# Optimization experiments

Hardware: AMD Instinct MI355X
Metric: run time of the kernel (lower is better)

## Reference

```python
import jax, jax.numpy as jnp
import numpy as np

B, L, D, H = 2, 128, 256, 256
BASE_LR = 0.01
LR_SHIFT = float(np.log(np.expm1(BASE_LR)))  # log(expm1(base_lr))


def silu_backward(x):
    s = jax.nn.silu(x)
    return s + jax.nn.sigmoid(x) * (1.0 - s)


def decay_matrix(log_g):
    # log_g: [B,L] -> M[b,l,m] = exp(sum_{i=m+1..l} log_g[b,i]) for m<=l, else 0
    n = log_g.shape[1]
    strict = jnp.tril(jnp.ones((n, n), log_g.dtype), -1)
    cum = jnp.cumsum(log_g[:, :, None] * strict, axis=1)
    return jnp.exp(cum) * jnp.tril(jnp.ones((n, n), log_g.dtype))


def setup_inputs():
    key = jax.random.key(0)
    ks = jax.random.split(key, 22)
    p = lambda k, shape: jax.random.normal(k, shape, jnp.float32) * 0.02
    inp = {
        'x': jax.random.normal(ks[0], (B, L, D), jnp.float32),
        'Wq': p(ks[1], (D, D)), 'bq': p(ks[2], (D,)),
        'Wk': p(ks[3], (D, D)), 'bk': p(ks[4], (D,)),
        'Wv': p(ks[5], (D, D)), 'bv': p(ks[6], (D,)),
        'Wlr': p(ks[7], (D, 1)), 'blr': p(ks[8], (1,)),
        'Wm': p(ks[9], (D, 1)), 'bm': p(ks[10], (1,)),
        'Wd': p(ks[11], (D, 1)), 'bd': p(ks[12], (1,)),
        'W1': p(ks[13], (B, H, D)), 'b1': p(ks[14], (B, H)),
        'W2': p(ks[15], (B, D, H)), 'b2': p(ks[16], (B, D)),
        'mW1': p(ks[17], (B, H, D)), 'mb1': p(ks[18], (B, H)),
        'mW2': p(ks[19], (B, D, H)), 'mb2': p(ks[20], (B, D)),
    }
    return inp


def reference(x, Wq, bq, Wk, bk, Wv, bv, Wlr, blr, Wm, bm, Wd, bd,
              W1, b1, W2, b2, mW1, mb1, mW2, mb2):
    query = x @ Wq + bq
    key_ = x @ Wk + bk
    value = x @ Wv + bv

    # forward through fast-weight MLP at current (chunk-start) weights
    Z1 = jnp.einsum('bhd,bld->blh', W1, key_) + b1[:, None, :]
    X2 = jax.nn.silu(Z1)
    Z2 = jnp.einsum('bdh,blh->bld', W2, X2) + b2[:, None, :]

    # per-token gradients of 0.5*||Z2 - value||^2
    grad_Z2 = Z2 - value
    grad_b2 = grad_Z2
    grad_W2 = jnp.einsum('bld,blh->bldh', grad_Z2, X2)
    grad_X2 = jnp.einsum('bld,bdh->blh', grad_Z2, W2)
    grad_Z1 = grad_X2 * silu_backward(Z1)
    grad_b1 = grad_Z1
    grad_W1 = jnp.einsum('blh,bld->blhd', grad_Z1, key_)

    lr = jax.nn.softplus((x @ Wlr).squeeze(-1) + blr + LR_SHIFT)  # [B,L]
    gW1 = grad_W1 * lr[:, :, None, None]
    gb1 = grad_b1 * lr[:, :, None]
    gW2 = grad_W2 * lr[:, :, None, None]
    gb2 = grad_b2 * lr[:, :, None]

    # momentum recurrence (decay-gated linear scan, materialized as LxL matrix)
    fc_mom = (x @ Wm).squeeze(-1) + bm  # [B,L]
    log_mom = -jax.nn.softplus(-fc_mom)
    M = decay_matrix(log_mom)  # [B,L,L]
    mom_cum = jnp.exp(jnp.cumsum(log_mom, axis=1))  # [B,L]

    mgW1 = jnp.einsum('blm,bmhd->blhd', M, gW1) - jnp.einsum('bl,bhd->blhd', mom_cum, mW1)
    mgb1 = jnp.einsum('blm,bmh->blh', M, gb1) - jnp.einsum('bl,bh->blh', mom_cum, mb1)
    mgW2 = jnp.einsum('blm,bmdh->bldh', M, gW2) - jnp.einsum('bl,bdh->bldh', mom_cum, mW2)
    mgb2 = jnp.einsum('blm,bmd->bld', M, gb2) - jnp.einsum('bl,bd->bld', mom_cum, mb2)

    # weight-decay recurrence
    log_wd = -jax.nn.softplus((x @ Wd).squeeze(-1) + bd)  # [B,L]
    Dm = decay_matrix(log_wd)
    wd_cum = jnp.exp(jnp.cumsum(log_wd, axis=1))

    W1p = jnp.einsum('blm,bmhd->blhd', Dm, mgW1) + jnp.einsum('bl,bhd->blhd', wd_cum, W1)
    b1p = jnp.einsum('blm,bmh->blh', Dm, mgb1) + jnp.einsum('bl,bh->blh', wd_cum, b1)
    W2p = jnp.einsum('blm,bmdh->bldh', Dm, mgW2) + jnp.einsum('bl,bdh->bldh', wd_cum, W2)
    b2p = jnp.einsum('blm,bmd->bld', Dm, mgb2) + jnp.einsum('bl,bd->bld', wd_cum, b2)

    # query pass through per-token updated weights
    Zq1 = jnp.einsum('blhd,bld->blh', W1p, query) + b1p
    Zq2 = jnp.einsum('bldh,blh->bld', W2p, jax.nn.silu(Zq1)) + b2p

    return (Zq2,
            W1p[:, -1], b1p[:, -1], W2p[:, -1], b2p[:, -1],
            mgW1[:, -1], mgb1[:, -1], mgW2[:, -1], mgb2[:, -1])
```

## Files before the change

### kernel.cpp

```cpp
#include <hip/hip_runtime.h>
#include <hip/hip_bf16.h>
#include <math.h>

constexpr int Bn = 2, Ln = 128, Dn = 256, Hn = 256;

#define LR_SHIFT (-4.6001660040607144f)

constexpr int OFF_Q      = 0;
constexpr int OFF_K      = 65536;
constexpr int OFF_V      = 131072;
constexpr int OFF_X2     = 196608;
constexpr int OFF_SILD   = 262144;
constexpr int OFF_XQ     = 327680;
constexpr int OFF_KT     = 393216;
constexpr int OFF_X2T    = 458752;
constexpr int OFF_A      = 524288;
constexpr int OFF_B1CAT  = 557056;
constexpr int OFF_B2CAT  = 884736;
constexpr int OFF_A1CAT  = 1212416;
constexpr int OFF_A2CAT  = 1376256;
constexpr int OFF_FC     = 1540096;
constexpr int OFF_LR     = 1540864;
constexpr int OFF_PM     = 1541120;
constexpr int OFF_PD     = 1541376;
constexpr int OFF_MOMCUM = 1541632;
constexpr int OFF_WDCUM  = 1541888;
constexpr int OFF_C      = 1542144;
constexpr int OFF_WCAT   = OFF_A1CAT;

constexpr int OUT_ZQ2  = 0;
constexpr int OUT_W1P  = 65536;
constexpr int OUT_B1P  = 196608;
constexpr int OUT_W2P  = 197120;
constexpr int OUT_B2P  = 328192;
constexpr int OUT_MGW1 = 328704;
constexpr int OUT_MGB1 = 459776;
constexpr int OUT_MGW2 = 460288;
constexpr int OUT_MGB2 = 591360;

__device__ __forceinline__ float softplus_f(float z) {
    return fmaxf(z, 0.0f) + log1pf(expf(-fabsf(z)));
}

__device__ __forceinline__ void gemm_mainloop(
    const float* __restrict__ A, int lda,
    const float* __restrict__ B, int ldb, int K,
    float4& c0, float4& c1) {
    __shared__ float As[32][34];
    __shared__ float Bs[32][64];
    const int t = threadIdx.x;
    const int tx = t & 15, ty = t >> 4;
    const int am = t >> 3, ak4 = (t & 7) << 2;
    const int bk = t >> 4, bn4 = (t & 15) << 2;
    c0 = make_float4(0.f, 0.f, 0.f, 0.f);
    c1 = make_float4(0.f, 0.f, 0.f, 0.f);
    for (int kc = 0; kc < K; kc += 32) {
        float4 ga  = *(const float4*)(A + am * lda + kc + ak4);
        float4 gb0 = *(const float4*)(B + (kc + bk) * ldb + bn4);
        float4 gb1 = *(const float4*)(B + (kc + bk + 16) * ldb + bn4);
        __syncthreads();
        As[ak4 + 0][am] = ga.x; As[ak4 + 1][am] = ga.y;
        As[ak4 + 2][am] = ga.z; As[ak4 + 3][am] = ga.w;
        *(float4*)&Bs[bk][bn4]      = gb0;
        *(float4*)&Bs[bk + 16][bn4] = gb1;
        __syncthreads();
#pragma unroll
        for (int k = 0; k < 32; ++k) {
            float a0 = As[k][2 * ty], a1 = As[k][2 * ty + 1];
            float4 b4 = *(const float4*)&Bs[k][4 * tx];
            c0.x += a0 * b4.x; c0.y += a0 * b4.y; c0.z += a0 * b4.z; c0.w += a0 * b4.w;
            c1.x += a1 * b4.x; c1.y += a1 * b4.y; c1.z += a1 * b4.z; c1.w += a1 * b4.w;
        }
    }
}

__global__ __launch_bounds__(256) void repack_kernel(
    const float* __restrict__ Wq, const float* __restrict__ Wk,
    const float* __restrict__ Wv, const float* __restrict__ Wlr,
    const float* __restrict__ Wm, const float* __restrict__ Wd,
    float* __restrict__ ws) {
    int d = blockIdx.x, t = threadIdx.x;
    float* row = ws + OFF_WCAT + d * 832;
    row[t]       = Wq[d * 256 + t];
    row[256 + t] = Wk[d * 256 + t];
    row[512 + t] = Wv[d * 256 + t];
    if (t == 0) { row[768] = Wlr[d]; row[769] = Wm[d]; row[770] = Wd[d]; }
    if (t < 61) row[771 + t] = 0.0f;
}

__global__ __launch_bounds__(256) void transpose_kernel(
    const float* __restrict__ W1, const float* __restrict__ W2,
    const float* __restrict__ mW1, const float* __restrict__ mW2,
    float* __restrict__ ws) {
    int z = blockIdx.z; int mat = z >> 1; int b = z & 1;
    const float* src; float* dst;
    if (mat == 0)      { src = W1  + b * 65536; dst = ws + OFF_B1CAT + b * 163840 + 128 * 256; }
    else if (mat == 1) { src = W2  + b * 65536; dst = ws + OFF_B2CAT + b * 163840 + 128 * 256; }
    else if (mat == 2) { src = mW1 + b * 65536; dst = ws + OFF_B1CAT + b * 163840 + 384 * 256; }
    else               { src = mW2 + b * 65536; dst = ws + OFF_B2CAT + b * 163840 + 384 * 256; }
    __shared__ float tile[32][33];
    int tx = threadIdx.x & 31, ty = threadIdx.x >> 5;
    int r0 = blockIdx.y * 32, c0 = blockIdx.x * 32;
    for (int i = 0; i < 32; i += 8)
        tile[ty + i][tx] = src[(r0 + ty + i) * 256 + (c0 + tx)];
    __syncthreads();
    for (int i = 0; i < 32; i += 8)
        dst[(c0 + ty + i) * 256 + (r0 + tx)] = tile[tx][ty + i];
}

__global__ __launch_bounds__(256) void qkv_kernel(
    const float* __restrict__ x, const float* __restrict__ bq,
    const float* __restrict__ bkb, const float* __restrict__ bv,
    float* __restrict__ ws) {
    int colT = blockIdx.x, rowT = blockIdx.y;
    const float* A = x + rowT * 32 * 256;
    const float* B = ws + OFF_WCAT + colT * 64;
    float4 c0, c1;
    gemm_mainloop(A, 256, B, 832, 256, c0, c1);
    int tx = threadIdx.x & 15, ty = threadIdx.x >> 4;
    float cc[2][4] = {{c0.x, c0.y, c0.z, c0.w}, {c1.x, c1.y, c1.z, c1.w}};
#pragma unroll
    for (int i = 0; i < 2; ++i)
#pragma unroll
        for (int j = 0; j < 4; ++j) {
            int m = rowT * 32 + 2 * ty + i;
            int c = colT * 64 + 4 * tx + j;
            float v = cc[i][j];
            if (c < 256) {
                ws[OFF_Q + m * 256 + c] = v + bq[c];
            } else if (c < 512) {
                int d = c - 256; float kv = v + bkb[d];
                ws[OFF_K + m * 256 + d] = kv;
                ws[OFF_KT + (m >> 7) * 32768 + d * 128 + (m & 127)] = kv;
            } else if (c < 768) {
                ws[OFF_V + m * 256 + (c - 512)] = v + bv[c - 512];
            } else if (c == 768) ws[OFF_FC + m] = v;
            else if (c == 769) ws[OFF_FC + 256 + m] = v;
            else if (c == 770) ws[OFF_FC + 512 + m] = v;
        }
}

__global__ __launch_bounds__(128) void scan_kernel(
    const float* __restrict__ blr, const float* __restrict__ bm,
    const float* __restrict__ bd, float* __restrict__ ws) {
    int b = blockIdx.x, t = threadIdx.x;
    int m = b * 128 + t;
    ws[OFF_LR + m] = softplus_f(ws[OFF_FC + m] + blr[0] + LR_SHIFT);
    float lm = -softplus_f(-(ws[OFF_FC + 256 + m] + bm[0]));
    float ld = -softplus_f(ws[OFF_FC + 512 + m] + bd[0]);
    __shared__ float sm[128], sd[128], se[128];
    sm[t] = lm; sd[t] = ld;
    __syncthreads();
    for (int off = 1; off < 128; off <<= 1) {
        float am = (t >= off) ? sm[t - off] : 0.0f;
        float ad = (t >= off) ? sd[t - off] : 0.0f;
        __syncthreads();
        sm[t] += am; sd[t] += ad;
        __syncthreads();
    }
    float pm = sm[t], pd = sd[t];
    ws[OFF_PM + m] = pm;
    ws[OFF_PD + m] = pd;
    ws[OFF_MOMCUM + m] = expf(pm);
    ws[OFF_WDCUM + m]  = expf(pd);
    se[t] = expf(pm - pd);
    __syncthreads();
    for (int off = 1; off < 128; off <<= 1) {
        float a = (t >= off) ? se[t - off] : 0.0f;
        __syncthreads();
        se[t] += a;
        __syncthreads();
    }
    ws[OFF_C + m] = expf(pd) * se[t];
}

__global__ __launch_bounds__(256) void a_kernel(float* __restrict__ ws) {
    int bl = blockIdx.x, b = bl >> 7, l = bl & 127, t = threadIdx.x;
    const float* Pm = ws + OFF_PM + b * 128;
    const float* Pd = ws + OFF_PD + b * 128;
    if (t < 128) {
        float a = 0.0f;
        if (t <= l) {
            float pdl = Pd[l], pmm1 = Pm[t], s = 0.0f;
            for (int mm = t; mm <= l; ++mm)
                s += expf((pdl - Pd[mm]) + (Pm[mm] - pmm1));
            a = s;
        }
        ws[OFF_A + bl * 128 + t] = a;
    }
    float q  = ws[OFF_Q + bl * 256 + t];
    float wd = ws[OFF_WDCUM + b * 128 + l];
    float cl = ws[OFF_C + b * 128 + l];
    float* A1 = ws + OFF_A1CAT + b * 81920 + l * 640;
    A1[128 + t] = wd * q;
    A1[384 + t] = -cl * q;
}

__global__ __launch_bounds__(256) void z1_kernel(
    const float* __restrict__ b1, float* __restrict__ ws) {
    int colT = blockIdx.x, rowT = blockIdx.y, b = blockIdx.z;
    const float* A = ws + OFF_K + b * 32768 + rowT * 32 * 256;
    const float* B = ws + OFF_B1CAT + b * 163840 + 128 * 256 + colT * 64;
    float4 c0, c1;
    gemm_mainloop(A, 256, B, 256, 256, c0, c1);
    int tx = threadIdx.x & 15, ty = threadIdx.x >> 4;
    float cc[2][4] = {{c0.x, c0.y, c0.z, c0.w}, {c1.x, c1.y, c1.z, c1.w}};
#pragma unroll
    for (int i = 0; i < 2; ++i)
#pragma unroll
        for (int j = 0; j < 4; ++j) {
            int ml = rowT * 32 + 2 * ty + i;
            int n = colT * 64 + 4 * tx + j;
            float z = cc[i][j] + b1[b * 256 + n];
            float sg = 1.0f / (1.0f + expf(-z));
            float x2 = z * sg;
            int gm = b * 128 + ml;
            ws[OFF_X2 + gm * 256 + n] = x2;
            ws[OFF_X2T + b * 32768 + n * 128 + ml] = x2;
            ws[OFF_SILD + gm * 256 + n] = x2 + sg * (1.0f - x2);
        }
}

__global__ __launch_bounds__(256) void z2_kernel(
    const float* __restrict__ b2, float* __restrict__ ws) {
    int colT = blockIdx.x, rowT = blockIdx.y, b = blockIdx.z;
    const float* A = ws + OFF_X2 + b * 32768 + rowT * 32 * 256;
    const float* B = ws + OFF_B2CAT + b * 163840 + 128 * 256 + colT * 64;
    float4 c0, c1;
    gemm_mainloop(A, 256, B, 256, 256, c0, c1);
    int tx = threadIdx.x & 15, ty = threadIdx.x >> 4;
    float cc[2][4] = {{c0.x, c0.y, c0.z, c0.w}, {c1.x, c1.y, c1.z, c1.w}};
#pragma unroll
    for (int i = 0; i < 2; ++i)
#pragma unroll
        for (int j = 0; j < 4; ++j) {
            int ml = rowT * 32 + 2 * ty + i;
            int n = colT * 64 + 4 * tx + j;
            int gm = b * 128 + ml;
            float gz2 = cc[i][j] + b2[b * 256 + n] - ws[OFF_V + gm * 256 + n];
            ws[OFF_B2CAT + b * 163840 + ml * 256 + n] = gz2;
        }
}

__global__ __launch_bounds__(256) void gx2_kernel(
    const float* __restrict__ W2, float* __restrict__ ws) {
    int colT = blockIdx.x, rowT = blockIdx.y, b = blockIdx.z;
    const float* A = ws + OFF_B2CAT + b * 163840 + rowT * 32 * 256;
    const float* B = W2 + b * 65536 + colT * 64;
    float4 c0, c1;
    gemm_mainloop(A, 256, B, 256, 256, c0, c1);
    int tx = threadIdx.x & 15, ty = threadIdx.x >> 4;
    float cc[2][4] = {{c0.x, c0.y, c0.z, c0.w}, {c1.x, c1.y, c1.z, c1.w}};
#pragma unroll
    for (int i = 0; i < 2; ++i)
#pragma unroll
        for (int j = 0; j < 4; ++j) {
            int ml = rowT * 32 + 2 * ty + i;
            int n = colT * 64 + 4 * tx + j;
            int gm = b * 128 + ml;
            float gz1 = cc[i][j] * ws[OFF_SILD + gm * 256 + n];
            ws[OFF_B1CAT + b * 163840 + ml * 256 + n] = gz1;
        }
}

__global__ __launch_bounds__(256) void score_kernel(
    const float* __restrict__ Arows, const float* __restrict__ Bt,
    float* __restrict__ Acat, const float* __restrict__ ws) {
    int colT = blockIdx.x, rowT = blockIdx.y, b = blockIdx.z;
    int tx = threadIdx.x & 15, ty = threadIdx.x >> 4;
    if (colT * 64 > rowT * 32 + 31) {
#pragma unroll
        for (int i = 0; i < 2; ++i)
#pragma unroll
            for (int j = 0; j < 4; ++j) {
                int l = rowT * 32 + 2 * ty + i;
                int mc = colT * 64 + 4 * tx + j;
                Acat[b * 81920 + l * 640 + mc] = 0.0f;
            }
        return;
    }
    const float* A = Arows + b * 32768 + rowT * 32 * 256;
    const float* B = Bt + b * 32768 + colT * 64;
    float4 c0, c1;
    gemm_mainloop(A, 256, B, 128, 256, c0, c1);
    float cc[2][4] = {{c0.x, c0.y, c0.z, c0.w}, {c1.x, c1.y, c1.z, c1.w}};
#pragma unroll
    for (int i = 0; i < 2; ++i)
#pragma unroll
        for (int j = 0; j < 4; ++j) {
            int l = rowT * 32 + 2 * ty + i;
            int mc = colT * 64 + 4 * tx + j;
            float p = 0.0f;
            if (mc <= l)
                p = ws[OFF_A + (b * 128 + l) * 128 + mc] *
                    ws[OFF_LR + b * 128 + mc] * (1.0f + cc[i][j]);
            Acat[b * 81920 + l * 640 + mc] = p;
        }
}

__global__ __launch_bounds__(256) void zq1_kernel(
    const float* __restrict__ b1, const float* __restrict__ mb1,
    float* __restrict__ ws) {
    int colT = blockIdx.x, rowT = blockIdx.y, b = blockIdx.z;
    const float* A = ws + OFF_A1CAT + b * 81920 + rowT * 32 * 640;
    const float* B = ws + OFF_B1CAT + b * 163840 + colT * 64;
    float4 c0, c1;
    gemm_mainloop(A, 640, B, 256, 640, c0, c1);
    int tx = threadIdx.x & 15, ty = threadIdx.x >> 4;
    float cc[2][4] = {{c0.x, c0.y, c0.z, c0.w}, {c1.x, c1.y, c1.z, c1.w}};
#pragma unroll
    for (int i = 0; i < 2; ++i)
#pragma unroll
        for (int j = 0; j < 4; ++j) {
            int ml = rowT * 32 + 2 * ty + i;
            int n = colT * 64 + 4 * tx + j;
            float cl = ws[OFF_C + b * 128 + ml];
            float wd = ws[OFF_WDCUM + b * 128 + ml];
            float z = cc[i][j] + wd * b1[b * 256 + n] - cl * mb1[b * 256 + n];
            float sg = 1.0f / (1.0f + expf(-z));
            float xq = z * sg;
            ws[OFF_XQ + (b * 128 + ml) * 256 + n] = xq;
            float* A2 = ws + OFF_A2CAT + b * 81920 + ml * 640;
            A2[128 + n] = wd * xq;
            A2[384 + n] = -cl * xq;
        }
}

__global__ __launch_bounds__(256) void zq2_kernel(
    const float* __restrict__ b2, const float* __restrict__ mb2,
    float* __restrict__ out, float* __restrict__ ws) {
    int colT = blockIdx.x, rowT = blockIdx.y, b = blockIdx.z;
    const float* A = ws + OFF_A2CAT + b * 81920 + rowT * 32 * 640;
    const float* B = ws + OFF_B2CAT + b * 163840 + colT * 64;
    float4 c0, c1;
    gemm_mainloop(A, 640, B, 256, 640, c0, c1);
    int tx = threadIdx.x & 15, ty = threadIdx.x >> 4;
    float cc[2][4] = {{c0.x, c0.y, c0.z, c0.w}, {c1.x, c1.y, c1.z, c1.w}};
#pragma unroll
    for (int i = 0; i < 2; ++i)
#pragma unroll
        for (int j = 0; j < 4; ++j) {
            int ml = rowT * 32 + 2 * ty + i;
            int n = colT * 64 + 4 * tx + j;
            float cl = ws[OFF_C + b * 128 + ml];
            float wd = ws[OFF_WDCUM + b * 128 + ml];
            out[OUT_ZQ2 + (b * 128 + ml) * 256 + n] =
                cc[i][j] + wd * b2[b * 256 + n] - cl * mb2[b * 256 + n];
        }
}

__global__ __launch_bounds__(256) void lastw_kernel(
    const float* __restrict__ W1, const float* __restrict__ mW1,
    const float* __restrict__ W2, const float* __restrict__ mW2,
    const float* __restrict__ ws, float* __restrict__ out) {
    int z = blockIdx.z; int b = z >> 1; int fam = z & 1;
    int t = threadIdx.x;
    __shared__ float wa[128], wm[128];
    __shared__ float LA[128][16], LM[128][16], R[128][16];
    const float* lr = ws + OFF_LR + b * 128;
    const float* Pm = ws + OFF_PM + b * 128;
    const float* Arow = ws + OFF_A + (b * 128 + 127) * 128;
    if (t < 128) {
        wa[t] = Arow[t] * lr[t];
        wm[t] = expf(Pm[127] - Pm[t]) * lr[t];
    }
    const float* left  = ws + (fam == 0 ? OFF_B1CAT : OFF_B2CAT) + b * 163840;
    const float* right = ws + (fam == 0 ? OFF_K : OFF_X2) + b * 32768;
    int i0 = blockIdx.y * 16, j0 = blockIdx.x * 16;
    __syncthreads();
    for (int e = t; e < 2048; e += 256) {
        int m = e >> 4, i = e & 15;
        float lv = left[m * 256 + i0 + i];
        LA[m][i] = wa[m] * lv;
        LM[m][i] = wm[m] * lv;
        R[m][i]  = right[m * 256 + j0 + i];
    }
    __syncthreads();
    int tx = t & 15, ty = t >> 4;
    float accA = 0.0f, accM = 0.0f;
#pragma unroll 4
    for (int m = 0; m < 128; ++m) {
        accA += LA[m][ty] * R[m][tx];
        accM += LM[m][ty] * R[m][tx];
    }
    float c_last  = ws[OFF_C + b * 128 + 127];
    float wd_last = ws[OFF_WDCUM + b * 128 + 127];
    float mc_last = ws[OFF_MOMCUM + b * 128 + 127];
    int i = i0 + ty, j = j0 + tx;
    const float* base1 = (fam == 0 ? W1 : W2) + b * 65536;
    const float* basem = (fam == 0 ? mW1 : mW2) + b * 65536;
    float b1v = base1[i * 256 + j], bmv = basem[i * 256 + j];
    int op = (fam == 0 ? OUT_W1P : OUT_W2P) + (b * 256 + i) * 256 + j;
    int om = (fam == 0 ? OUT_MGW1 : OUT_MGW2) + (b * 256 + i) * 256 + j;
    out[op] = accA - c_last * bmv + wd_last * b1v;
    out[om] = accM - mc_last * bmv;
}

__global__ __launch_bounds__(256) void lastb_kernel(
    const float* __restrict__ b1, const float* __restrict__ mb1,
    const float* __restrict__ b2, const float* __restrict__ mb2,
    const float* __restrict__ ws, float* __restrict__ out) {
    int b = blockIdx.x; int t = threadIdx.x;
    __shared__ float wa[128], wm[128];
    if (t < 128) {
        wa[t] = ws[OFF_A + (b * 128 + 127) * 128 + t] * ws[OFF_LR + b * 128 + t];
        wm[t] = expf(ws[OFF_PM + b * 128 + 127] - ws[OFF_PM + b * 128 + t]) *
                ws[OFF_LR + b * 128 + t];
    }
    __syncthreads();
    const float* gz1 = ws + OFF_B1CAT + b * 163840;
    const float* gz2 = ws + OFF_B2CAT + b * 163840;
    float sA1 = 0, sM1 = 0, sA2 = 0, sM2 = 0;
#pragma unroll 4
    for (int m = 0; m < 128; ++m) {
        float g1 = gz1[m * 256 + t], g2 = gz2[m * 256 + t];
        sA1 += wa[m] * g1; sM1 += wm[m] * g1;
        sA2 += wa[m] * g2; sM2 += wm[m] * g2;
    }
    float c_last  = ws[OFF_C + b * 128 + 127];
    float wd_last = ws[OFF_WDCUM + b * 128 + 127];
    float mc_last = ws[OFF_MOMCUM + b * 128 + 127];
    out[OUT_B1P + b * 256 + t]  = sA1 - c_last * mb1[b * 256 + t] + wd_last * b1[b * 256 + t];
    out[OUT_MGB1 + b * 256 + t] = sM1 - mc_last * mb1[b * 256 + t];
    out[OUT_B2P + b * 256 + t]  = sA2 - c_last * mb2[b * 256 + t] + wd_last * b2[b * 256 + t];
    out[OUT_MGB2 + b * 256 + t] = sM2 - mc_last * mb2[b * 256 + t];
}

extern "C" void kernel_launch(void* const* d_in, const int* in_sizes, int n_in,
                              void* d_out, int out_size, void* d_ws, size_t ws_size,
                              hipStream_t stream) {
    const float* x   = (const float*)d_in[0];
    const float* Wq  = (const float*)d_in[1];
    const float* bq  = (const float*)d_in[2];
    const float* Wk  = (const float*)d_in[3];
    const float* bk  = (const float*)d_in[4];
    const float* Wv  = (const float*)d_in[5];
    const float* bv  = (const float*)d_in[6];
    const float* Wlr = (const float*)d_in[7];
    const float* blr = (const float*)d_in[8];
    const float* Wm  = (const float*)d_in[9];
    const float* bm  = (const float*)d_in[10];
    const float* Wd  = (const float*)d_in[11];
    const float* bd  = (const float*)d_in[12];
    const float* W1  = (const float*)d_in[13];
    const float* b1  = (const float*)d_in[14];
    const float* W2  = (const float*)d_in[15];
    const float* b2  = (const float*)d_in[16];
    const float* mW1 = (const float*)d_in[17];
    const float* mb1 = (const float*)d_in[18];
    const float* mW2 = (const float*)d_in[19];
    const float* mb2 = (const float*)d_in[20];
    float* ws  = (float*)d_ws;
    float* out = (float*)d_out;

    repack_kernel<<<256, 256, 0, stream>>>(Wq, Wk, Wv, Wlr, Wm, Wd, ws);
    transpose_kernel<<<dim3(8, 8, 8), 256, 0, stream>>>(W1, W2, mW1, mW2, ws);
    qkv_kernel<<<dim3(13, 8), 256, 0, stream>>>(x, bq, bk, bv, ws);
    scan_kernel<<<Bn, 128, 0, stream>>>(blr, bm, bd, ws);
    a_kernel<<<Bn * Ln, 256, 0, stream>>>(ws);
    z1_kernel<<<dim3(4, 4, Bn), 256, 0, stream>>>(b1, ws);
    z2_kernel<<<dim3(4, 4, Bn), 256, 0, stream>>>(b2, ws);
    gx2_kernel<<<dim3(4, 4, Bn), 256, 0, stream>>>(W2, ws);
    score_kernel<<<dim3(2, 4, Bn), 256, 0, stream>>>(ws + OFF_Q, ws + OFF_KT,
                                                     ws + OFF_A1CAT, ws);
    zq1_kernel<<<dim3(4, 4, Bn), 256, 0, stream>>>(b1, mb1, ws);
    score_kernel<<<dim3(2, 4, Bn), 256, 0, stream>>>(ws + OFF_XQ, ws + OFF_X2T,
                                                     ws + OFF_A2CAT, ws);
    zq2_kernel<<<dim3(4, 4, Bn), 256, 0, stream>>>(b2, mb2, out, ws);
    lastw_kernel<<<dim3(16, 16, Bn * 2), 256, 0, stream>>>(W1, mW1, W2, mW2, ws, out);
    lastb_kernel<<<Bn, 256, 0, stream>>>(b1, mb1, b2, mb2, ws, out);
}
```

Measured before the change: 250.6 us.

## Fuse all stages into one persistent kernel with software grid barriers

Replaces the chain of fourteen small kernel launches with a single persistent 256-block kernel. Stages are separated by an atomic grid barrier, and independent work such as the last-weight reductions is spread across otherwise idle blocks alongside the dependent GEMM stages. The aim is to remove launch overhead and inter-kernel gaps, which dominate for these tiny GEMMs. The lastw job is also retiled to 32x32 tiles with a 2x2 register block. The code assumes all 256 blocks are co-resident; if they are not, the barrier deadlocks, and each barrier adds its own spin latency.

```diff
diff --git a/kernel.cpp b/kernel.cpp
--- a/kernel.cpp
+++ b/kernel.cpp
@@ -1,8 +1,7 @@
 #include <hip/hip_runtime.h>
-#include <hip/hip_bf16.h>
 #include <math.h>
 
-constexpr int Bn = 2, Ln = 128, Dn = 256, Hn = 256;
+constexpr int Bn = 2, Ln = 128;
 
 #define LR_SHIFT (-4.6001660040607144f)
 
@@ -26,7 +25,7 @@
 constexpr int OFF_MOMCUM = 1541632;
 constexpr int OFF_WDCUM  = 1541888;
 constexpr int OFF_C      = 1542144;
-constexpr int OFF_WCAT   = OFF_A1CAT;
+constexpr int OFF_BAR    = 1542656;
 
 constexpr int OUT_ZQ2  = 0;
 constexpr int OUT_W1P  = 65536;
@@ -38,16 +37,41 @@
 constexpr int OUT_MGW2 = 460288;
 constexpr int OUT_MGB2 = 591360;
 
+constexpr int NBLK = 256;
+
 __device__ __forceinline__ float softplus_f(float z) {
     return fmaxf(z, 0.0f) + log1pf(expf(-fabsf(z)));
 }
 
-__device__ __forceinline__ void gemm_mainloop(
-    const float* __restrict__ A, int lda,
-    const float* __restrict__ B, int ldb, int K,
-    float4& c0, float4& c1) {
-    __shared__ float As[32][34];
-    __shared__ float Bs[32][64];
+__device__ __forceinline__ float dot4(float4 a, float4 b) {
+    return a.x * b.x + a.y * b.y + a.z * b.z + a.w * b.w;
+}
+
+__device__ __forceinline__ void grid_barrier(unsigned* bar) {
+    __syncthreads();
+    if (threadIdx.x == 0) {
+        unsigned* cnt = bar;
+        unsigned* gen = bar + 1;
+        unsigned g = __hip_atomic_load(gen, __ATOMIC_ACQUIRE, __HIP_MEMORY_SCOPE_AGENT);
+        unsigned arrived = __hip_atomic_fetch_add(cnt, 1u, __ATOMIC_ACQ_REL,
+                                                  __HIP_MEMORY_SCOPE_AGENT);
+        if (arrived == (unsigned)NBLK - 1) {
+            __hip_atomic_store(cnt, 0u, __ATOMIC_RELAXED, __HIP_MEMORY_SCOPE_AGENT);
+            __hip_atomic_fetch_add(gen, 1u, __ATOMIC_ACQ_REL, __HIP_MEMORY_SCOPE_AGENT);
+        } else {
+            while (__hip_atomic_load(gen, __ATOMIC_ACQUIRE,
+                                     __HIP_MEMORY_SCOPE_AGENT) == g)
+                __builtin_amdgcn_s_sleep(8);
+        }
+    }
+    __syncthreads();
+}
+
+__device__ __forceinline__ void gemm_tile(
+    const float* A, int lda, const float* B, int ldb, int K,
+    float* smem, float4& c0, float4& c1) {
+    float (*As)[34] = (float(*)[34])smem;
+    float (*Bs)[64] = (float(*)[64])(smem + 1088);
     const int t = threadIdx.x;
     const int tx = t & 15, ty = t >> 4;
     const int am = t >> 3, ak4 = (t & 7) << 2;
@@ -74,356 +98,415 @@
     }
 }
 
-__global__ __launch_bounds__(256) void repack_kernel(
-    const float* __restrict__ Wq, const float* __restrict__ Wk,
-    const float* __restrict__ Wv, const float* __restrict__ Wlr,
-    const float* __restrict__ Wm, const float* __restrict__ Wd,
-    float* __restrict__ ws) {
-    int d = blockIdx.x, t = threadIdx.x;
-    float* row = ws + OFF_WCAT + d * 832;
-    row[t]       = Wq[d * 256 + t];
-    row[256 + t] = Wk[d * 256 + t];
-    row[512 + t] = Wv[d * 256 + t];
-    if (t == 0) { row[768] = Wlr[d]; row[769] = Wm[d]; row[770] = Wd[d]; }
-    if (t < 61) row[771 + t] = 0.0f;
-}
-
-__global__ __launch_bounds__(256) void transpose_kernel(
-    const float* __restrict__ W1, const float* __restrict__ W2,
-    const float* __restrict__ mW1, const float* __restrict__ mW2,
-    float* __restrict__ ws) {
-    int z = blockIdx.z; int mat = z >> 1; int b = z & 1;
-    const float* src; float* dst;
-    if (mat == 0)      { src = W1  + b * 65536; dst = ws + OFF_B1CAT + b * 163840 + 128 * 256; }
-    else if (mat == 1) { src = W2  + b * 65536; dst = ws + OFF_B2CAT + b * 163840 + 128 * 256; }
-    else if (mat == 2) { src = mW1 + b * 65536; dst = ws + OFF_B1CAT + b * 163840 + 384 * 256; }
-    else               { src = mW2 + b * 65536; dst = ws + OFF_B2CAT + b * 163840 + 384 * 256; }
-    __shared__ float tile[32][33];
-    int tx = threadIdx.x & 31, ty = threadIdx.x >> 5;
-    int r0 = blockIdx.y * 32, c0 = blockIdx.x * 32;
-    for (int i = 0; i < 32; i += 8)
-        tile[ty + i][tx] = src[(r0 + ty + i) * 256 + (c0 + tx)];
+__device__ __forceinline__ void lastw_job(
+    int b, int fam, int i0, int j0,
+    const float* W1, const float* mW1, const float* W2, const float* mW2,
+    float* ws, float* out, float* smem) {
+    const int t = threadIdx.x;
+    float* wa = smem;
+    float* wm = smem + 128;
+    float (*Ls)[36] = (float(*)[36])(smem + 256);
+    float (*Rs)[36] = (float(*)[36])(smem + 256 + 1152);
     __syncthreads();
-    for (int i = 0; i < 32; i += 8)
-        dst[(c0 + ty + i) * 256 + (r0 + tx)] = tile[tx][ty + i];
-}
-
-__global__ __launch_bounds__(256) void qkv_kernel(
-    const float* __restrict__ x, const float* __restrict__ bq,
-    const float* __restrict__ bkb, const float* __restrict__ bv,
-    float* __restrict__ ws) {
-    int colT = blockIdx.x, rowT = blockIdx.y;
-    const float* A = x + rowT * 32 * 256;
-    const float* B = ws + OFF_WCAT + colT * 64;
-    float4 c0, c1;
-    gemm_mainloop(A, 256, B, 832, 256, c0, c1);
-    int tx = threadIdx.x & 15, ty = threadIdx.x >> 4;
-    float cc[2][4] = {{c0.x, c0.y, c0.z, c0.w}, {c1.x, c1.y, c1.z, c1.w}};
-#pragma unroll
-    for (int i = 0; i < 2; ++i)
-#pragma unroll
-        for (int j = 0; j < 4; ++j) {
-            int m = rowT * 32 + 2 * ty + i;
-            int c = colT * 64 + 4 * tx + j;
-            float v = cc[i][j];
-            if (c < 256) {
-                ws[OFF_Q + m * 256 + c] = v + bq[c];
-            } else if (c < 512) {
-                int d = c - 256; float kv = v + bkb[d];
-                ws[OFF_K + m * 256 + d] = kv;
-                ws[OFF_KT + (m >> 7) * 32768 + d * 128 + (m & 127)] = kv;
-            } else if (c < 768) {
-                ws[OFF_V + m * 256 + (c - 512)] = v + bv[c - 512];
-            } else if (c == 768) ws[OFF_FC + m] = v;
-            else if (c == 769) ws[OFF_FC + 256 + m] = v;
-            else if (c == 770) ws[OFF_FC + 512 + m] = v;
-        }
-}
-
-__global__ __launch_bounds__(128) void scan_kernel(
-    const float* __restrict__ blr, const float* __restrict__ bm,
-    const float* __restrict__ bd, float* __restrict__ ws) {
-    int b = blockIdx.x, t = threadIdx.x;
-    int m = b * 128 + t;
-    ws[OFF_LR + m] = softplus_f(ws[OFF_FC + m] + blr[0] + LR_SHIFT);
-    float lm = -softplus_f(-(ws[OFF_FC + 256 + m] + bm[0]));
-    float ld = -softplus_f(ws[OFF_FC + 512 + m] + bd[0]);
-    __shared__ float sm[128], sd[128], se[128];
-    sm[t] = lm; sd[t] = ld;
-    __syncthreads();
-    for (int off = 1; off < 128; off <<= 1) {
-        float am = (t >= off) ? sm[t - off] : 0.0f;
-        float ad = (t >= off) ? sd[t - off] : 0.0f;
-        __syncthreads();
-        sm[t] += am; sd[t] += ad;
-        __syncthreads();
-    }
-    float pm = sm[t], pd = sd[t];
-    ws[OFF_PM + m] = pm;
-    ws[OFF_PD + m] = pd;
-    ws[OFF_MOMCUM + m] = expf(pm);
-    ws[OFF_WDCUM + m]  = expf(pd);
-    se[t] = expf(pm - pd);
-    __syncthreads();
-    for (int off = 1; off < 128; off <<= 1) {
-        float a = (t >= off) ? se[t - off] : 0.0f;
-        __syncthreads();
-        se[t] += a;
-        __syncthreads();
-    }
-    ws[OFF_C + m] = expf(pd) * se[t];
-}
-
-__global__ __launch_bounds__(256) void a_kernel(float* __restrict__ ws) {
-    int bl = blockIdx.x, b = bl >> 7, l = bl & 127, t = threadIdx.x;
-    const float* Pm = ws + OFF_PM + b * 128;
-    const float* Pd = ws + OFF_PD + b * 128;
     if (t < 128) {
-        float a = 0.0f;
-        if (t <= l) {
-            float pdl = Pd[l], pmm1 = Pm[t], s = 0.0f;
-            for (int mm = t; mm <= l; ++mm)
-                s += expf((pdl - Pd[mm]) + (Pm[mm] - pmm1));
-            a = s;
-        }
-        ws[OFF_A + bl * 128 + t] = a;
-    }
-    float q  = ws[OFF_Q + bl * 256 + t];
-    float wd = ws[OFF_WDCUM + b * 128 + l];
-    float cl = ws[OFF_C + b * 128 + l];
-    float* A1 = ws + OFF_A1CAT + b * 81920 + l * 640;
-    A1[128 + t] = wd * q;
-    A1[384 + t] = -cl * q;
-}
-
-__global__ __launch_bounds__(256) void z1_kernel(
-    const float* __restrict__ b1, float* __restrict__ ws) {
-    int colT = blockIdx.x, rowT = blockIdx.y, b = blockIdx.z;
-    const float* A = ws + OFF_K + b * 32768 + rowT * 32 * 256;
-    const float* B = ws + OFF_B1CAT + b * 163840 + 128 * 256 + colT * 64;
-    float4 c0, c1;
-    gemm_mainloop(A, 256, B, 256, 256, c0, c1);
-    int tx = threadIdx.x & 15, ty = threadIdx.x >> 4;
-    float cc[2][4] = {{c0.x, c0.y, c0.z, c0.w}, {c1.x, c1.y, c1.z, c1.w}};
-#pragma unroll
-    for (int i = 0; i < 2; ++i)
-#pragma unroll
-        for (int j = 0; j < 4; ++j) {
-            int ml = rowT * 32 + 2 * ty + i;
-            int n = colT * 64 + 4 * tx + j;
-            float z = cc[i][j] + b1[b * 256 + n];
-            float sg = 1.0f / (1.0f + expf(-z));
-            float x2 = z * sg;
-            int gm = b * 128 + ml;
-            ws[OFF_X2 + gm * 256 + n] = x2;
-            ws[OFF_X2T + b * 32768 + n * 128 + ml] = x2;
-            ws[OFF_SILD + gm * 256 + n] = x2 + sg * (1.0f - x2);
-        }
-}
-
-__global__ __launch_bounds__(256) void z2_kernel(
-    const float* __restrict__ b2, float* __restrict__ ws) {
-    int colT = blockIdx.x, rowT = blockIdx.y, b = blockIdx.z;
-    const float* A = ws + OFF_X2 + b * 32768 + rowT * 32 * 256;
-    const float* B = ws + OFF_B2CAT + b * 163840 + 128 * 256 + colT * 64;
-    float4 c0, c1;
-    gemm_mainloop(A, 256, B, 256, 256, c0, c1);
-    int tx = threadIdx.x & 15, ty = threadIdx.x >> 4;
-    float cc[2][4] = {{c0.x, c0.y, c0.z, c0.w}, {c1.x, c1.y, c1.z, c1.w}};
-#pragma unroll
-    for (int i = 0; i < 2; ++i)
-#pragma unroll
-        for (int j = 0; j < 4; ++j) {
-            int ml = rowT * 32 + 2 * ty + i;
-            int n = colT * 64 + 4 * tx + j;
-            int gm = b * 128 + ml;
-            float gz2 = cc[i][j] + b2[b * 256 + n] - ws[OFF_V + gm * 256 + n];
-            ws[OFF_B2CAT + b * 163840 + ml * 256 + n] = gz2;
-        }
-}
-
-__global__ __launch_bounds__(256) void gx2_kernel(
-    const float* __restrict__ W2, float* __restrict__ ws) {
-    int colT = blockIdx.x, rowT = blockIdx.y, b = blockIdx.z;
-    const float* A = ws + OFF_B2CAT + b * 163840 + rowT * 32 * 256;
-    const float* B = W2 + b * 65536 + colT * 64;
-    float4 c0, c1;
-    gemm_mainloop(A, 256, B, 256, 256, c0, c1);
-    int tx = threadIdx.x & 15, ty = threadIdx.x >> 4;
-    float cc[2][4] = {{c0.x, c0.y, c0.z, c0.w}, {c1.x, c1.y, c1.z, c1.w}};
-#pragma unroll
-    for (int i = 0; i < 2; ++i)
-#pragma unroll
-        for (int j = 0; j < 4; ++j) {
-            int ml = rowT * 32 + 2 * ty + i;
-            int n = colT * 64 + 4 * tx + j;
-            int gm = b * 128 + ml;
-            float gz1 = cc[i][j] * ws[OFF_SILD + gm * 256 + n];
-            ws[OFF_B1CAT + b * 163840 + ml * 256 + n] = gz1;
-        }
-}
-
-__global__ __launch_bounds__(256) void score_kernel(
-    const float* __restrict__ Arows, const float* __restrict__ Bt,
-    float* __restrict__ Acat, const float* __restrict__ ws) {
-    int colT = blockIdx.x, rowT = blockIdx.y, b = blockIdx.z;
-    int tx = threadIdx.x & 15, ty = threadIdx.x >> 4;
-    if (colT * 64 > rowT * 32 + 31) {
-#pragma unroll
-        for (int i = 0; i < 2; ++i)
-#pragma unroll
-            for (int j = 0; j < 4; ++j) {
-                int l = rowT * 32 + 2 * ty + i;
-                int mc = colT * 64 + 4 * tx + j;
-                Acat[b * 81920 + l * 640 + mc] = 0.0f;
-            }
-        return;
-    }
-    const float* A = Arows + b * 32768 + rowT * 32 * 256;
-    const float* B = Bt + b * 32768 + colT * 64;
-    float4 c0, c1;
-    gemm_mainloop(A, 256, B, 128, 256, c0, c1);
-    float cc[2][4] = {{c0.x, c0.y, c0.z, c0.w}, {c1.x, c1.y, c1.z, c1.w}};
-#pragma unroll
-    for (int i = 0; i < 2; ++i)
-#pragma unroll
-        for (int j = 0; j < 4; ++j) {
-            int l = rowT * 32 + 2 * ty + i;
-            int mc = colT * 64 + 4 * tx + j;
-            float p = 0.0f;
-            if (mc <= l)
-                p = ws[OFF_A + (b * 128 + l) * 128 + mc] *
-                    ws[OFF_LR + b * 128 + mc] * (1.0f + cc[i][j]);
-            Acat[b * 81920 + l * 640 + mc] = p;
-        }
-}
-
-__global__ __launch_bounds__(256) void zq1_kernel(
-    const float* __restrict__ b1, const float* __restrict__ mb1,
-    float* __restrict__ ws) {
-    int colT = blockIdx.x, rowT = blockIdx.y, b = blockIdx.z;
-    const float* A = ws + OFF_A1CAT + b * 81920 + rowT * 32 * 640;
-    const float* B = ws + OFF_B1CAT + b * 163840 + colT * 64;
-    float4 c0, c1;
-    gemm_mainloop(A, 640, B, 256, 640, c0, c1);
-    int tx = threadIdx.x & 15, ty = threadIdx.x >> 4;
-    float cc[2][4] = {{c0.x, c0.y, c0.z, c0.w}, {c1.x, c1.y, c1.z, c1.w}};
-#pragma unroll
-    for (int i = 0; i < 2; ++i)
-#pragma unroll
-        for (int j = 0; j < 4; ++j) {
-            int ml = rowT * 32 + 2 * ty + i;
-            int n = colT * 64 + 4 * tx + j;
-            float cl = ws[OFF_C + b * 128 + ml];
-            float wd = ws[OFF_WDCUM + b * 128 + ml];
-            float z = cc[i][j] + wd * b1[b * 256 + n] - cl * mb1[b * 256 + n];
-            float sg = 1.0f / (1.0f + expf(-z));
-            float xq = z * sg;
-            ws[OFF_XQ + (b * 128 + ml) * 256 + n] = xq;
-            float* A2 = ws + OFF_A2CAT + b * 81920 + ml * 640;
-            A2[128 + n] = wd * xq;
-            A2[384 + n] = -cl * xq;
-        }
-}
-
-__global__ __launch_bounds__(256) void zq2_kernel(
-    const float* __restrict__ b2, const float* __restrict__ mb2,
-    float* __restrict__ out, float* __restrict__ ws) {
-    int colT = blockIdx.x, rowT = blockIdx.y, b = blockIdx.z;
-    const float* A = ws + OFF_A2CAT + b * 81920 + rowT * 32 * 640;
-    const float* B = ws + OFF_B2CAT + b * 163840 + colT * 64;
-    float4 c0, c1;
-    gemm_mainloop(A, 640, B, 256, 640, c0, c1);
-    int tx = threadIdx.x & 15, ty = threadIdx.x >> 4;
-    float cc[2][4] = {{c0.x, c0.y, c0.z, c0.w}, {c1.x, c1.y, c1.z, c1.w}};
-#pragma unroll
-    for (int i = 0; i < 2; ++i)
-#pragma unroll
-        for (int j = 0; j < 4; ++j) {
-            int ml = rowT * 32 + 2 * ty + i;
-            int n = colT * 64 + 4 * tx + j;
-            float cl = ws[OFF_C + b * 128 + ml];
-            float wd = ws[OFF_WDCUM + b * 128 + ml];
-            out[OUT_ZQ2 + (b * 128 + ml) * 256 + n] =
-                cc[i][j] + wd * b2[b * 256 + n] - cl * mb2[b * 256 + n];
-        }
-}
-
-__global__ __launch_bounds__(256) void lastw_kernel(
-    const float* __restrict__ W1, const float* __restrict__ mW1,
-    const float* __restrict__ W2, const float* __restrict__ mW2,
-    const float* __restrict__ ws, float* __restrict__ out) {
-    int z = blockIdx.z; int b = z >> 1; int fam = z & 1;
-    int t = threadIdx.x;
-    __shared__ float wa[128], wm[128];
-    __shared__ float LA[128][16], LM[128][16], R[128][16];
-    const float* lr = ws + OFF_LR + b * 128;
-    const float* Pm = ws + OFF_PM + b * 128;
-    const float* Arow = ws + OFF_A + (b * 128 + 127) * 128;
-    if (t < 128) {
-        wa[t] = Arow[t] * lr[t];
-        wm[t] = expf(Pm[127] - Pm[t]) * lr[t];
-    }
-    const float* left  = ws + (fam == 0 ? OFF_B1CAT : OFF_B2CAT) + b * 163840;
-    const float* right = ws + (fam == 0 ? OFF_K : OFF_X2) + b * 32768;
-    int i0 = blockIdx.y * 16, j0 = blockIdx.x * 16;
-    __syncthreads();
-    for (int e = t; e < 2048; e += 256) {
-        int m = e >> 4, i = e & 15;
-        float lv = left[m * 256 + i0 + i];
-        LA[m][i] = wa[m] * lv;
-        LM[m][i] = wm[m] * lv;
-        R[m][i]  = right[m * 256 + j0 + i];
-    }
-    __syncthreads();
+        float lrv = ws[OFF_LR + b * 128 + t];
+        wa[t] = ws[OFF_A + (b * 128 + 127) * 128 + t] * lrv;
+        wm[t] = expf(ws[OFF_PM + b * 128 + 127] - ws[OFF_PM + b * 128 + t]) * lrv;
+    }
+    const float* left  = ws + (fam ? OFF_B2CAT : OFF_B1CAT) + b * 163840;
+    const float* right = ws + (fam ? OFF_X2 : OFF_K) + b * 32768;
+    float accA[2][2] = {{0.f, 0.f}, {0.f, 0.f}};
+    float accM[2][2] = {{0.f, 0.f}, {0.f, 0.f}};
     int tx = t & 15, ty = t >> 4;
-    float accA = 0.0f, accM = 0.0f;
-#pragma unroll 4
-    for (int m = 0; m < 128; ++m) {
-        accA += LA[m][ty] * R[m][tx];
-        accM += LM[m][ty] * R[m][tx];
+    int lrow = t >> 3, lc4 = (t & 7) << 2;
+    for (int kc = 0; kc < 128; kc += 32) {
+        __syncthreads();
+        *(float4*)&Ls[lrow][lc4] = *(const float4*)(left + (kc + lrow) * 256 + i0 + lc4);
+        *(float4*)&Rs[lrow][lc4] = *(const float4*)(right + (kc + lrow) * 256 + j0 + lc4);
+        __syncthreads();
+#pragma unroll
+        for (int k = 0; k < 32; ++k) {
+            float wak = wa[kc + k], wmk = wm[kc + k];
+            float l0 = Ls[k][2 * ty], l1 = Ls[k][2 * ty + 1];
+            float r0 = Rs[k][2 * tx], r1 = Rs[k][2 * tx + 1];
+            float p00 = l0 * r0, p01 = l0 * r1, p10 = l1 * r0, p11 = l1 * r1;
+            accA[0][0] += wak * p00; accA[0][1] += wak * p01;
+            accA[1][0] += wak * p10; accA[1][1] += wak * p11;
+            accM[0][0] += wmk * p00; accM[0][1] += wmk * p01;
+            accM[1][0] += wmk * p10; accM[1][1] += wmk * p11;
+        }
     }
     float c_last  = ws[OFF_C + b * 128 + 127];
     float wd_last = ws[OFF_WDCUM + b * 128 + 127];
     float mc_last = ws[OFF_MOMCUM + b * 128 + 127];
-    int i = i0 + ty, j = j0 + tx;
-    const float* base1 = (fam == 0 ? W1 : W2) + b * 65536;
-    const float* basem = (fam == 0 ? mW1 : mW2) + b * 65536;
-    float b1v = base1[i * 256 + j], bmv = basem[i * 256 + j];
-    int op = (fam == 0 ? OUT_W1P : OUT_W2P) + (b * 256 + i) * 256 + j;
-    int om = (fam == 0 ? OUT_MGW1 : OUT_MGW2) + (b * 256 + i) * 256 + j;
-    out[op] = accA - c_last * bmv + wd_last * b1v;
-    out[om] = accM - mc_last * bmv;
-}
-
-__global__ __launch_bounds__(256) void lastb_kernel(
-    const float* __restrict__ b1, const float* __restrict__ mb1,
-    const float* __restrict__ b2, const float* __restrict__ mb2,
-    const float* __restrict__ ws, float* __restrict__ out) {
-    int b = blockIdx.x; int t = threadIdx.x;
-    __shared__ float wa[128], wm[128];
-    if (t < 128) {
-        wa[t] = ws[OFF_A + (b * 128 + 127) * 128 + t] * ws[OFF_LR + b * 128 + t];
-        wm[t] = expf(ws[OFF_PM + b * 128 + 127] - ws[OFF_PM + b * 128 + t]) *
-                ws[OFF_LR + b * 128 + t];
-    }
-    __syncthreads();
-    const float* gz1 = ws + OFF_B1CAT + b * 163840;
-    const float* gz2 = ws + OFF_B2CAT + b * 163840;
-    float sA1 = 0, sM1 = 0, sA2 = 0, sM2 = 0;
+    const float* base1 = (fam ? W2 : W1) + b * 65536;
+    const float* basem = (fam ? mW2 : mW1) + b * 65536;
+    int opB = fam ? OUT_W2P : OUT_W1P;
+    int omB = fam ? OUT_MGW2 : OUT_MGW1;
+#pragma unroll
+    for (int di = 0; di < 2; ++di)
+#pragma unroll
+        for (int dj = 0; dj < 2; ++dj) {
+            int i = i0 + 2 * ty + di, j = j0 + 2 * tx + dj;
+            float b1v = base1[i * 256 + j], bmv = basem[i * 256 + j];
+            out[opB + (b * 256 + i) * 256 + j] = accA[di][dj] - c_last * bmv + wd_last * b1v;
+            out[omB + (b * 256 + i) * 256 + j] = accM[di][dj] - mc_last * bmv;
+        }
+}
+
+__global__ __launch_bounds__(256) void fused_kernel(
+    const float* x,
+    const float* Wq, const float* bq,
+    const float* Wk, const float* bk,
+    const float* Wv, const float* bv,
+    const float* Wlr, const float* blr,
+    const float* Wm, const float* bm,
+    const float* Wd, const float* bd,
+    const float* W1, const float* b1,
+    const float* W2, const float* b2,
+    const float* mW1, const float* mb1,
+    const float* mW2, const float* mb2,
+    float* ws, float* out) {
+    __shared__ float smem[3136];
+    const int bid = blockIdx.x;
+    const int t = threadIdx.x;
+    const int tx = t & 15, ty = t >> 4;
+    unsigned* bar = (unsigned*)(ws + OFF_BAR);
+
+    for (int j = bid; j < 616; j += NBLK) {
+        __syncthreads();
+        if (j < 96) {
+            int which = j / 32, tile = j % 32, rowT = tile >> 2, colT = tile & 3;
+            const float* Wp = which == 0 ? Wq : (which == 1 ? Wk : Wv);
+            const float* bp = which == 0 ? bq : (which == 1 ? bk : bv);
+            float4 c0, c1;
+            gemm_tile(x + rowT * 32 * 256, 256, Wp + colT * 64, 256, 256, smem, c0, c1);
+            float cc[2][4] = {{c0.x, c0.y, c0.z, c0.w}, {c1.x, c1.y, c1.z, c1.w}};
+#pragma unroll
+            for (int i = 0; i < 2; ++i)
+#pragma unroll
+                for (int jj = 0; jj < 4; ++jj) {
+                    int m = rowT * 32 + 2 * ty + i;
+                    int c = colT * 64 + 4 * tx + jj;
+                    float v = cc[i][jj] + bp[c];
+                    if (which == 0) {
+                        ws[OFF_Q + m * 256 + c] = v;
+                    } else if (which == 1) {
+                        ws[OFF_K + m * 256 + c] = v;
+                        ws[OFF_KT + (m >> 7) * 32768 + c * 128 + (m & 127)] = v;
+                    } else {
+                        ws[OFF_V + m * 256 + c] = v;
+                    }
+                }
+        } else if (j < 104) {
+            int tk0 = (j - 96) * 32;
+            float* ww = smem;
+            ww[t] = Wlr[t]; ww[256 + t] = Wm[t]; ww[512 + t] = Wd[t];
+            __syncthreads();
+            int wv = t >> 6, lane = t & 63;
+            float4 wl = *(const float4*)(ww + lane * 4);
+            float4 wmv = *(const float4*)(ww + 256 + lane * 4);
+            float4 wdv = *(const float4*)(ww + 512 + lane * 4);
+            for (int i = 0; i < 8; ++i) {
+                int tok = tk0 + wv * 8 + i;
+                float4 xv = *(const float4*)(x + tok * 256 + lane * 4);
+                float d0 = dot4(xv, wl), d1 = dot4(xv, wmv), d2 = dot4(xv, wdv);
+#pragma unroll
+                for (int off = 32; off > 0; off >>= 1) {
+                    d0 += __shfl_down(d0, off);
+                    d1 += __shfl_down(d1, off);
+                    d2 += __shfl_down(d2, off);
+                }
+                if (lane == 0) {
+                    ws[OFF_FC + tok] = d0;
+                    ws[OFF_FC + 256 + tok] = d1;
+                    ws[OFF_FC + 512 + tok] = d2;
+                }
+            }
+        } else {
+            int j2 = j - 104;
+            int mat = j2 >> 7, rem = j2 & 127, b = rem >> 6, tile = rem & 63;
+            int r0 = (tile >> 3) * 32, c0 = (tile & 7) * 32;
+            const float* src; float* dst;
+            if (mat == 0)      { src = W1  + b * 65536; dst = ws + OFF_B1CAT + b * 163840 + 128 * 256; }
+            else if (mat == 1) { src = W2  + b * 65536; dst = ws + OFF_B2CAT + b * 163840 + 128 * 256; }
+            else if (mat == 2) { src = mW1 + b * 65536; dst = ws + OFF_B1CAT + b * 163840 + 384 * 256; }
+            else               { src = mW2 + b * 65536; dst = ws + OFF_B2CAT + b * 163840 + 384 * 256; }
+            float (*tl)[33] = (float(*)[33])smem;
+            int ttx = t & 31, tty = t >> 5;
+#pragma unroll
+            for (int i = 0; i < 32; i += 8)
+                tl[tty + i][ttx] = src[(r0 + tty + i) * 256 + (c0 + ttx)];
+            __syncthreads();
+#pragma unroll
+            for (int i = 0; i < 32; i += 8)
+                dst[(c0 + tty + i) * 256 + (r0 + ttx)] = tl[ttx][tty + i];
+        }
+    }
+    grid_barrier(bar);
+
+    if (bid < 32) {
+        int b = bid >> 4, tile = bid & 15, rowT = tile >> 2, colT = tile & 3;
+        float4 c0, c1;
+        gemm_tile(ws + OFF_K + b * 32768 + rowT * 32 * 256, 256,
+                  ws + OFF_B1CAT + b * 163840 + 128 * 256 + colT * 64, 256, 256,
+                  smem, c0, c1);
+        float cc[2][4] = {{c0.x, c0.y, c0.z, c0.w}, {c1.x, c1.y, c1.z, c1.w}};
+#pragma unroll
+        for (int i = 0; i < 2; ++i)
+#pragma unroll
+            for (int jj = 0; jj < 4; ++jj) {
+                int ml = rowT * 32 + 2 * ty + i;
+                int n = colT * 64 + 4 * tx + jj;
+                float z = cc[i][jj] + b1[b * 256 + n];
+                float sg = 1.0f / (1.0f + expf(-z));
+                float x2 = z * sg;
+                int gm = b * 128 + ml;
+                ws[OFF_X2 + gm * 256 + n] = x2;
+                ws[OFF_X2T + b * 32768 + n * 128 + ml] = x2;
+                ws[OFF_SILD + gm * 256 + n] = x2 + sg * (1.0f - x2);
+            }
+    } else if (bid == 32) {
+        int i = t & 127;
+        float* sm = smem; float* sd = smem + 256; float* se = smem + 512;
+        ws[OFF_LR + t] = softplus_f(ws[OFF_FC + t] + blr[0] + LR_SHIFT);
+        float lm = -softplus_f(-(ws[OFF_FC + 256 + t] + bm[0]));
+        float ld = -softplus_f(ws[OFF_FC + 512 + t] + bd[0]);
+        sm[t] = lm; sd[t] = ld;
+        __syncthreads();
+        for (int off = 1; off < 128; off <<= 1) {
+            float am_ = (i >= off) ? sm[t - off] : 0.0f;
+            float ad_ = (i >= off) ? sd[t - off] : 0.0f;
+            __syncthreads();
+            sm[t] += am_; sd[t] += ad_;
+            __syncthreads();
+        }
+        float pm = sm[t], pd = sd[t];
+        ws[OFF_PM + t] = pm;
+        ws[OFF_PD + t] = pd;
+        ws[OFF_MOMCUM + t] = expf(pm);
+        ws[OFF_WDCUM + t] = expf(pd);
+        se[t] = expf(pm - pd);
+        __syncthreads();
+        for (int off = 1; off < 128; off <<= 1) {
+            float a_ = (i >= off) ? se[t - off] : 0.0f;
+            __syncthreads();
+            se[t] += a_;
+            __syncthreads();
+        }
+        ws[OFF_C + t] = expf(pd) * se[t];
+    }
+    grid_barrier(bar);
+
+    for (int j = bid; j < 288; j += NBLK) {
+        __syncthreads();
+        if (j < 32) {
+            int b = j >> 4, tile = j & 15, rowT = tile >> 2, colT = tile & 3;
+            float4 c0, c1;
+            gemm_tile(ws + OFF_X2 + b * 32768 + rowT * 32 * 256, 256,
+                      ws + OFF_B2CAT + b * 163840 + 128 * 256 + colT * 64, 256, 256,
+                      smem, c0, c1);
+            float cc[2][4] = {{c0.x, c0.y, c0.z, c0.w}, {c1.x, c1.y, c1.z, c1.w}};
+#pragma unroll
+            for (int i = 0; i < 2; ++i)
+#pragma unroll
+                for (int jj = 0; jj < 4; ++jj) {
+                    int ml = rowT * 32 + 2 * ty + i;
+                    int n = colT * 64 + 4 * tx + jj;
+                    int gm = b * 128 + ml;
+                    float gz2 = cc[i][jj] + b2[b * 256 + n] - ws[OFF_V + gm * 256 + n];
+                    ws[OFF_B2CAT + b * 163840 + ml * 256 + n] = gz2;
+                }
+        } else {
+            int bl = j - 32, b = bl >> 7, l = bl & 127;
+            if (t < 128) {
+                float a = 0.0f;
+                if (t <= l) {
+                    const float* Pm = ws + OFF_PM + b * 128;
+                    const float* Pd = ws + OFF_PD + b * 128;
+                    float pdl = Pd[l], pmm = Pm[t], s = 0.0f;
+                    for (int mm = t; mm <= l; ++mm)
+                        s += expf((pdl - Pd[mm]) + (Pm[mm] - pmm));
+                    a = s;
+                }
+                ws[OFF_A + bl * 128 + t] = a;
+            }
+            float q  = ws[OFF_Q + bl * 256 + t];
+            float wdv = ws[OFF_WDCUM + b * 128 + l];
+            float cl = ws[OFF_C + b * 128 + l];
+            float* A1 = ws + OFF_A1CAT + b * 81920 + l * 640;
+            A1[128 + t] = wdv * q;
+            A1[384 + t] = -cl * q;
+        }
+    }
+    grid_barrier(bar);
+
+    if (bid < 32) {
+        int b = bid >> 4, tile = bid & 15, rowT = tile >> 2, colT = tile & 3;
+        float4 c0, c1;
+        gemm_tile(ws + OFF_B2CAT + b * 163840 + rowT * 32 * 256, 256,
+                  W2 + b * 65536 + colT * 64, 256, 256, smem, c0, c1);
+        float cc[2][4] = {{c0.x, c0.y, c0.z, c0.w}, {c1.x, c1.y, c1.z, c1.w}};
+#pragma unroll
+        for (int i = 0; i < 2; ++i)
+#pragma unroll
+            for (int jj = 0; jj < 4; ++jj) {
+                int ml = rowT * 32 + 2 * ty + i;
+                int n = colT * 64 + 4 * tx + jj;
+                int gm = b * 128 + ml;
+                float gz1 = cc[i][jj] * ws[OFF_SILD + gm * 256 + n];
+                ws[OFF_B1CAT + b * 163840 + ml * 256 + n] = gz1;
+            }
+    } else if (bid < 160) {
+        int jdx = bid - 32, b = jdx >> 6, tile = jdx & 63;
+        lastw_job(b, 1, (tile >> 3) * 32, (tile & 7) * 32,
+                  W1, mW1, W2, mW2, ws, out, smem);
+    }
+    grid_barrier(bar);
+
+    if (bid < 16) {
+        int b = bid >> 3, rowT = (bid >> 1) & 3, colT = bid & 1;
+        float* Acat = ws + OFF_A1CAT;
+        if (colT * 64 > rowT * 32 + 31) {
+#pragma unroll
+            for (int i = 0; i < 2; ++i)
+#pragma unroll
+                for (int jj = 0; jj < 4; ++jj) {
+                    int l = rowT * 32 + 2 * ty + i;
+                    int mc = colT * 64 + 4 * tx + jj;
+                    Acat[b * 81920 + l * 640 + mc] = 0.0f;
+                }
+        } else {
+            float4 c0, c1;
+            gemm_tile(ws + OFF_Q + b * 32768 + rowT * 32 * 256, 256,
+                      ws + OFF_KT + b * 32768 + colT * 64, 128, 256, smem, c0, c1);
+            float cc[2][4] = {{c0.x, c0.y, c0.z, c0.w}, {c1.x, c1.y, c1.z, c1.w}};
+#pragma unroll
+            for (int i = 0; i < 2; ++i)
+#pragma unroll
+                for (int jj = 0; jj < 4; ++jj) {
+                    int l = rowT * 32 + 2 * ty + i;
+                    int mc = colT * 64 + 4 * tx + jj;
+                    float p = 0.0f;
+                    if (mc <= l)
+                        p = ws[OFF_A + (b * 128 + l) * 128 + mc] *
+                            ws[OFF_LR + b * 128 + mc] * (1.0f + cc[i][jj]);
+                    Acat[b * 81920 + l * 640 + mc] = p;
+                }
+        }
+    } else if (bid < 144) {
+        int jdx = bid - 16, b = jdx >> 6, tile = jdx & 63;
+        lastw_job(b, 0, (tile >> 3) * 32, (tile & 7) * 32,
+                  W1, mW1, W2, mW2, ws, out, smem);
+    } else if (bid < 146) {
+        int b = bid - 144;
+        float* wa = smem; float* wm = smem + 128;
+        if (t < 128) {
+            float lrv = ws[OFF_LR + b * 128 + t];
+            wa[t] = ws[OFF_A + (b * 128 + 127) * 128 + t] * lrv;
+            wm[t] = expf(ws[OFF_PM + b * 128 + 127] - ws[OFF_PM + b * 128 + t]) * lrv;
+        }
+        __syncthreads();
+        const float* gz1 = ws + OFF_B1CAT + b * 163840;
+        const float* gz2 = ws + OFF_B2CAT + b * 163840;
+        float sA1 = 0, sM1 = 0, sA2 = 0, sM2 = 0;
 #pragma unroll 4
-    for (int m = 0; m < 128; ++m) {
-        float g1 = gz1[m * 256 + t], g2 = gz2[m * 256 + t];
-        sA1 += wa[m] * g1; sM1 += wm[m] * g1;
-        sA2 += wa[m] * g2; sM2 += wm[m] * g2;
-    }
-    float c_last  = ws[OFF_C + b * 128 + 127];
-    float wd_last = ws[OFF_WDCUM + b * 128 + 127];
-    float mc_last = ws[OFF_MOMCUM + b * 128 + 127];
-    out[OUT_B1P + b * 256 + t]  = sA1 - c_last * mb1[b * 256 + t] + wd_last * b1[b * 256 + t];
-    out[OUT_MGB1 + b * 256 + t] = sM1 - mc_last * mb1[b * 256 + t];
-    out[OUT_B2P + b * 256 + t]  = sA2 - c_last * mb2[b * 256 + t] + wd_last * b2[b * 256 + t];
-    out[OUT_MGB2 + b * 256 + t] = sM2 - mc_last * mb2[b * 256 + t];
+        for (int m = 0; m < 128; ++m) {
+            float g1 = gz1[m * 256 + t], g2 = gz2[m * 256 + t];
+            sA1 += wa[m] * g1; sM1 += wm[m] * g1;
+            sA2 += wa[m] * g2; sM2 += wm[m] * g2;
+        }
+        float c_last  = ws[OFF_C + b * 128 + 127];
+        float wd_last = ws[OFF_WDCUM + b * 128 + 127];
+        float mc_last = ws[OFF_MOMCUM + b * 128 + 127];
+        out[OUT_B1P + b * 256 + t]  = sA1 - c_last * mb1[b * 256 + t] + wd_last * b1[b * 256 + t];
+        out[OUT_MGB1 + b * 256 + t] = sM1 - mc_last * mb1[b * 256 + t];
+        out[OUT_B2P + b * 256 + t]  = sA2 - c_last * mb2[b * 256 + t] + wd_last * b2[b * 256 + t];
+        out[OUT_MGB2 + b * 256 + t] = sM2 - mc_last * mb2[b * 256 + t];
+    }
+    grid_barrier(bar);
+
+    if (bid < 32) {
+        int b = bid >> 4, tile = bid & 15, rowT = tile >> 2, colT = tile & 3;
+        float4 c0, c1;
+        gemm_tile(ws + OFF_A1CAT + b * 81920 + rowT * 32 * 640, 640,
+                  ws + OFF_B1CAT + b * 163840 + colT * 64, 256, 640, smem, c0, c1);
+        float cc[2][4] = {{c0.x, c0.y, c0.z, c0.w}, {c1.x, c1.y, c1.z, c1.w}};
+#pragma unroll
+        for (int i = 0; i < 2; ++i)
+#pragma unroll
+            for (int jj = 0; jj < 4; ++jj) {
+                int ml = rowT * 32 + 2 * ty + i;
+                int n = colT * 64 + 4 * tx + jj;
+                float cl = ws[OFF_C + b * 128 + ml];
+                float wdv = ws[OFF_WDCUM + b * 128 + ml];
+                float z = cc[i][jj] + wdv * b1[b * 256 + n] - cl * mb1[b * 256 + n];
+                float sg = 1.0f / (1.0f + expf(-z));
+                float xq = z * sg;
+                ws[OFF_XQ + (b * 128 + ml) * 256 + n] = xq;
+                float* A2 = ws + OFF_A2CAT + b * 81920 + ml * 640;
+                A2[128 + n] = wdv * xq;
+                A2[384 + n] = -cl * xq;
+            }
+    }
+    grid_barrier(bar);
+
+    if (bid < 16) {
+        int b = bid >> 3, rowT = (bid >> 1) & 3, colT = bid & 1;
+        float* Acat = ws + OFF_A2CAT;
+        if (colT * 64 > rowT * 32 + 31) {
+#pragma unroll
+            for (int i = 0; i < 2; ++i)
+#pragma unroll
+                for (int jj = 0; jj < 4; ++jj) {
+                    int l = rowT * 32 + 2 * ty + i;
+                    int mc = colT * 64 + 4 * tx + jj;
+                    Acat[b * 81920 + l * 640 + mc] = 0.0f;
+                }
+        } else {
+            float4 c0, c1;
+            gemm_tile(ws + OFF_XQ + b * 32768 + rowT * 32 * 256, 256,
+                      ws + OFF_X2T + b * 32768 + colT * 64, 128, 256, smem, c0, c1);
+            float cc[2][4] = {{c0.x, c0.y, c0.z, c0.w}, {c1.x, c1.y, c1.z, c1.w}};
+#pragma unroll
+            for (int i = 0; i < 2; ++i)
+#pragma unroll
+                for (int jj = 0; jj < 4; ++jj) {
+                    int l = rowT * 32 + 2 * ty + i;
+                    int mc = colT * 64 + 4 * tx + jj;
+                    float p = 0.0f;
+                    if (mc <= l)
+                        p = ws[OFF_A + (b * 128 + l) * 128 + mc] *
+                            ws[OFF_LR + b * 128 + mc] * (1.0f + cc[i][jj]);
+                    Acat[b * 81920 + l * 640 + mc] = p;
+                }
+        }
+    }
+    grid_barrier(bar);
+
+    if (bid < 32) {
+        int b = bid >> 4, tile = bid & 15, rowT = tile >> 2, colT = tile & 3;
+        float4 c0, c1;
+        gemm_tile(ws + OFF_A2CAT + b * 81920 + rowT * 32 * 640, 640,
+                  ws + OFF_B2CAT + b * 163840 + colT * 64, 256, 640, smem, c0, c1);
+        float cc[2][4] = {{c0.x, c0.y, c0.z, c0.w}, {c1.x, c1.y, c1.z, c1.w}};
+#pragma unroll
+        for (int i = 0; i < 2; ++i)
+#pragma unroll
+            for (int jj = 0; jj < 4; ++jj) {
+                int ml = rowT * 32 + 2 * ty + i;
+                int n = colT * 64 + 4 * tx + jj;
+                float cl = ws[OFF_C + b * 128 + ml];
+                float wdv = ws[OFF_WDCUM + b * 128 + ml];
+                out[OUT_ZQ2 + (b * 128 + ml) * 256 + n] =
+                    cc[i][jj] + wdv * b2[b * 256 + n] - cl * mb2[b * 256 + n];
+            }
+    }
+}
+
+__global__ void init_kernel(unsigned* bar) {
+    bar[0] = 0u;
+    bar[1] = 0u;
 }
 
 extern "C" void kernel_launch(void* const* d_in, const int* in_sizes, int n_in,
@@ -453,20 +536,8 @@
     float* ws  = (float*)d_ws;
     float* out = (float*)d_out;
 
-    repack_kernel<<<256, 256, 0, stream>>>(Wq, Wk, Wv, Wlr, Wm, Wd, ws);
-    transpose_kernel<<<dim3(8, 8, 8), 256, 0, stream>>>(W1, W2, mW1, mW2, ws);
-    qkv_kernel<<<dim3(13, 8), 256, 0, stream>>>(x, bq, bk, bv, ws);
-    scan_kernel<<<Bn, 128, 0, stream>>>(blr, bm, bd, ws);
-    a_kernel<<<Bn * Ln, 256, 0, stream>>>(ws);
-    z1_kernel<<<dim3(4, 4, Bn), 256, 0, stream>>>(b1, ws);
-    z2_kernel<<<dim3(4, 4, Bn), 256, 0, stream>>>(b2, ws);
-    gx2_kernel<<<dim3(4, 4, Bn), 256, 0, stream>>>(W2, ws);
-    score_kernel<<<dim3(2, 4, Bn), 256, 0, stream>>>(ws + OFF_Q, ws + OFF_KT,
-                                                     ws + OFF_A1CAT, ws);
-    zq1_kernel<<<dim3(4, 4, Bn), 256, 0, stream>>>(b1, mb1, ws);
-    score_kernel<<<dim3(2, 4, Bn), 256, 0, stream>>>(ws + OFF_XQ, ws + OFF_X2T,
-                                                     ws + OFF_A2CAT, ws);
-    zq2_kernel<<<dim3(4, 4, Bn), 256, 0, stream>>>(b2, mb2, out, ws);
-    lastw_kernel<<<dim3(16, 16, Bn * 2), 256, 0, stream>>>(W1, mW1, W2, mW2, ws, out);
-    lastb_kernel<<<Bn, 256, 0, stream>>>(b1, mb1, b2, mb2, ws, out);
-}
+    init_kernel<<<1, 1, 0, stream>>>((unsigned*)(ws + OFF_BAR));
+    fused_kernel<<<NBLK, 256, 0, stream>>>(
+        x, Wq, bq, Wk, bk, Wv, bv, Wlr, blr, Wm, bm, Wd, bd,
+        W1, b1, W2, b2, mW1, mb1, mW2, mb2, ws, out);
+}
```

After: 495.1 us. +97.6%, slower.
